# Optimization experiments

Measured on AMD Instinct MI355X. Metric: run time of the kernel, lower is better.

## Reference

```python
import math
import jax, jax.numpy as jnp
import numpy as np

B, S, D, H = 1, 4096, 1024, 16
HD = D // H


def setup_inputs() -> dict:
    key = jax.random.key(0)
    ks = jax.random.split(key, 11)
    s = 0.02
    inp = {
        "q": jax.random.normal(ks[0], (B, S, D), jnp.float32),
        "k": jax.random.normal(ks[1], (B, S, D), jnp.float32),
        "v": jax.random.normal(ks[2], (B, S, D), jnp.float32),
        # causal boolean mask, broadcastable over [B, H, S, S]
        "mask": jnp.tril(jnp.ones((S, S), jnp.bool_))[None, None],
        "Wq": jax.random.normal(ks[3], (D, D), jnp.float32) * s,
        "bq": jnp.zeros((D,), jnp.float32),
        "Wk": jax.random.normal(ks[4], (D, D), jnp.float32) * s,
        "bk": jnp.zeros((D,), jnp.float32),
        "Wv": jax.random.normal(ks[5], (D, D), jnp.float32) * s,
        "bv": jnp.zeros((D,), jnp.float32),
        "Wo": jax.random.normal(ks[6], (D, D), jnp.float32) * s,
        "bo": jnp.zeros((D,), jnp.float32),
    }
    return inp


def reference(q, k, v, mask, Wq, bq, Wk, bk, Wv, bv, Wo, bo):
    # projections (torch Linear: x @ W.T + b; here W is stored already transposed)
    qp = (q @ Wq + bq).reshape(B, S, H, HD)
    kp = (k @ Wk + bk).reshape(B, S, H, HD)
    vp = (v @ Wv + bv).reshape(B, S, H, HD)
    # scores: [B, H, S, S]
    scores = jnp.einsum("bqhd,bkhd->bhqk", qp, kp) / math.sqrt(HD)
    scores = jnp.where(mask, scores, -jnp.inf)
    attn = jax.nn.softmax(scores, axis=-1)
    # context: [B, H, S, HD] -> [B, S, D]
    ctx = jnp.einsum("bhqk,bkhd->bqhd", attn, vp).reshape(B, S, D)
    return ctx @ Wo + bo
```

## Files before the change

kernel.cpp:

```cpp
#include <hip/hip_runtime.h>
#include <hip/hip_bf16.h>


#define S_LEN 4096
#define D_DIM 1024
#define NHEAD 16
#define HDIM  64

typedef __hip_bfloat16 bf16;
typedef __attribute__((ext_vector_type(8))) short bf16x8v;
typedef __attribute__((ext_vector_type(4))) float f32x4;
typedef __attribute__((ext_vector_type(2))) unsigned int u32x2;

#define MFMA16(a, b, c) __builtin_amdgcn_mfma_f32_16x16x32_bf16((a), (b), (c), 0, 0, 0)

#if __has_builtin(__builtin_amdgcn_exp2f)
#define EXP2F(x) __builtin_amdgcn_exp2f(x)
#else
#define EXP2F(x) exp2f(x)
#endif

#define QSCALE (0.125f * 1.4426950408889634f)

__device__ __forceinline__ void async_cp16(const void* g, void* l) {
    __builtin_amdgcn_global_load_lds(
        (const __attribute__((address_space(1))) unsigned int*)g,
        (__attribute__((address_space(3))) unsigned int*)l, 16, 0, 0);
}

__device__ __forceinline__ unsigned int cvtpk_bf16(float lo, float hi) {
    unsigned int r;
    asm("v_cvt_pk_bf16_f32 %0, %1, %2" : "=v"(r) : "v"(lo), "v"(hi));
    return r;
}

__global__ __launch_bounds__(256) void cvt_bf16_k(
    const float* __restrict__ x0, const float* __restrict__ x1,
    const float* __restrict__ x2,
    bf16* __restrict__ y0, bf16* __restrict__ y1, bf16* __restrict__ y2)
{
    const float* x = (blockIdx.z == 0) ? x0 : (blockIdx.z == 1) ? x1 : x2;
    bf16*       y = (blockIdx.z == 0) ? y0 : (blockIdx.z == 1) ? y1 : y2;
    const size_t i = ((size_t)blockIdx.x * 256 + threadIdx.x);
    const float4 v = ((const float4*)x)[i];
    union { bf16 h[4]; short4 s; } u;
    u.h[0] = __float2bfloat16(v.x);
    u.h[1] = __float2bfloat16(v.y);
    u.h[2] = __float2bfloat16(v.z);
    u.h[3] = __float2bfloat16(v.w);
    ((short4*)y)[i] = u.s;
}

__global__ __launch_bounds__(256) void transpose_cvt_k(
    const float* __restrict__ W0, const float* __restrict__ W1,
    const float* __restrict__ W2, const float* __restrict__ W3,
    bf16* __restrict__ T0, bf16* __restrict__ T1,
    bf16* __restrict__ T2, bf16* __restrict__ T3)
{
    const float* W = (blockIdx.z == 0) ? W0 : (blockIdx.z == 1) ? W1
                   : (blockIdx.z == 2) ? W2 : W3;
    bf16*       Wt = (blockIdx.z == 0) ? T0 : (blockIdx.z == 1) ? T1
                   : (blockIdx.z == 2) ? T2 : T3;
    __shared__ float t[32][33];
    const int bx = blockIdx.x << 5, by = blockIdx.y << 5;
    const int tx = threadIdx.x & 31, ty = threadIdx.x >> 5;
#pragma unroll
    for (int i = 0; i < 32; i += 8)
        t[ty + i][tx] = W[(size_t)(by + ty + i) * D_DIM + bx + tx];
    __syncthreads();
#pragma unroll
    for (int i = 0; i < 32; i += 8)
        Wt[(size_t)(bx + ty + i) * D_DIM + by + tx] = __float2bfloat16(t[tx][ty + i]);
}

struct GemmJob {
    const bf16* A; const bf16* Wt; const float* bias; void* out;
    int mode; float scale;
};

__global__ __launch_bounds__(256) void gemm_k(GemmJob j0, GemmJob j1, GemmJob j2)
{
    const GemmJob j = (blockIdx.z == 0) ? j0 : (blockIdx.z == 1) ? j1 : j2;
    const int K = D_DIM;
    const int bn = blockIdx.x << 6;
    const int bm = blockIdx.y << 7;
    const int tid = threadIdx.x;
    const int w = tid >> 6, lane = tid & 63;
    const int col = lane & 15, g = lane >> 4;
    const int wr = (w >> 1) << 6, wc = (w & 1) << 5;

    __shared__ bf16 As[128 * 64];
    __shared__ bf16 Bs[64 * 64];

    f32x4 acc[4][2];
#pragma unroll
    for (int i = 0; i < 4; ++i)
#pragma unroll
        for (int jj = 0; jj < 2; ++jj) acc[i][jj] = (f32x4){0.f, 0.f, 0.f, 0.f};

    for (int kb = 0; kb < K; kb += 64) {
        __syncthreads();
#pragma unroll
        for (int e = 0; e < 4; ++e) {
            const int lin = (e << 8) + tid;
            const int row = lin >> 3, kc = lin & 7;
            async_cp16(j.A + (size_t)(bm + row) * K + kb + (kc << 3), &As[lin << 3]);
        }
#pragma unroll
        for (int e = 0; e < 2; ++e) {
            const int lin = (e << 8) + tid;
            const int row = lin >> 3, kc = lin & 7;
            async_cp16(j.Wt + (size_t)(bn + row) * K + kb + (kc << 3), &Bs[lin << 3]);
        }
        __syncthreads();

#pragma unroll
        for (int s = 0; s < 2; ++s) {
            bf16x8v af[4], bfv[2];
#pragma unroll
            for (int i = 0; i < 4; ++i)
                af[i] = *(const bf16x8v*)&As[((wr + (i << 4) + col) << 6) + (s << 5) + (g << 3)];
#pragma unroll
            for (int jj = 0; jj < 2; ++jj)
                bfv[jj] = *(const bf16x8v*)&Bs[((wc + (jj << 4) + col) << 6) + (s << 5) + (g << 3)];
#pragma unroll
            for (int i = 0; i < 4; ++i)
#pragma unroll
                for (int jj = 0; jj < 2; ++jj)
                    acc[i][jj] = MFMA16(af[i], bfv[jj], acc[i][jj]);
        }
    }

#pragma unroll
    for (int i = 0; i < 4; ++i)
#pragma unroll
    for (int jj = 0; jj < 2; ++jj)
#pragma unroll
    for (int reg = 0; reg < 4; ++reg) {
        const int row = bm + wr + (i << 4) + (g << 2) + reg;
        const int cg  = bn + wc + (jj << 4) + col;
        const float vv = (acc[i][jj][reg] + j.bias[cg]) * j.scale;
        if (j.mode == 0)
            ((bf16*)j.out)[(((size_t)(cg >> 6)) * S_LEN + row) * HDIM + (cg & 63)] =
                __float2bfloat16(vv);
        else if (j.mode == 2)
            ((bf16*)j.out)[((size_t)(cg >> 6) * HDIM + (cg & 63)) * S_LEN + row] =
                __float2bfloat16(vv);
        else
            ((float*)j.out)[(size_t)row * D_DIM + cg] = vv;
    }
}

__global__ __launch_bounds__(256) void attn_mfma_k(
    const bf16* __restrict__ Qp, const bf16* __restrict__ Kp,
    const bf16* __restrict__ Vt, bf16* __restrict__ ctx)
{
    __shared__ bf16 Ks[2][4096];
    __shared__ bf16 Vs[2][4096];

    const int bid = blockIdx.x;
    const int qb  = 31 - (bid >> 4);
    const int h   = bid & 15;
    const int q0  = qb << 7;
    const int tid = threadIdx.x, w = tid >> 6, lane = tid & 63;
    const int col = lane & 15, g = lane >> 4;

    const bf16* Kh = Kp + (size_t)h * S_LEN * HDIM;
    const bf16* Vh = Vt + (size_t)h * HDIM * S_LEN;

    const int qrowA = q0 + (w << 4) + col;
    const int qrowB = qrowA + 64;
    const size_t qbaseA = ((size_t)h * S_LEN + qrowA) * HDIM + (g << 3);
    const size_t qbaseB = qbaseA + (size_t)64 * HDIM;
    const bf16x8v qfA0 = *(const bf16x8v*)(Qp + qbaseA);
    const bf16x8v qfA1 = *(const bf16x8v*)(Qp + qbaseA + 32);
    const bf16x8v qfB0 = *(const bf16x8v*)(Qp + qbaseB);
    const bf16x8v qfB1 = *(const bf16x8v*)(Qp + qbaseB + 32);

    float plA = 0.f, plB = 0.f;
    f32x4 accA[4], accB[4];
#pragma unroll
    for (int t = 0; t < 4; ++t) {
        accA[t] = (f32x4){0.f, 0.f, 0.f, 0.f};
        accB[t] = (f32x4){0.f, 0.f, 0.f, 0.f};
    }

    const int nkb = (qb << 1) + 2;

    auto stage = [&](int buf, int kb) {
        const int kk0 = kb << 6;
#pragma unroll
        for (int e = 0; e < 2; ++e) {
            const int lin = (e << 8) + tid;
            const int t = lin >> 7, G = (lin >> 4) & 7, c = lin & 15;
            async_cp16(Kh + (size_t)(kk0 + (t << 4) + c) * HDIM + (G << 3),
                       &Ks[buf][lin << 3]);
            async_cp16(Vh + (size_t)((t << 4) + c) * S_LEN + kk0 + (G << 3),
                       &Vs[buf][lin << 3]);
        }
    };

    stage(0, 0);
    __syncthreads();

    for (int kb = 0; kb < nkb; ++kb) {
        const int cur = kb & 1;
        if (kb + 1 < nkb) stage(cur ^ 1, kb + 1);
        const int kk0 = kb << 6;
        const bf16* Kc = Ks[cur];
        const bf16* Vc = Vs[cur];

        f32x4 saA[4], saB[4];
#pragma unroll
        for (int t = 0; t < 4; ++t) {
            saA[t] = (f32x4){0.f, 0.f, 0.f, 0.f};
            saB[t] = (f32x4){0.f, 0.f, 0.f, 0.f};
        }
        __builtin_amdgcn_s_setprio(1);
#pragma unroll
        for (int t = 0; t < 4; ++t) {
            const bf16x8v kf0 = *(const bf16x8v*)&Kc[((t << 7) + (g << 4) + col) << 3];
            const bf16x8v kf1 = *(const bf16x8v*)&Kc[((t << 7) + 64 + (g << 4) + col) << 3];
            saA[t] = MFMA16(kf0, qfA0, saA[t]);
            saA[t] = MFMA16(kf1, qfA1, saA[t]);
            saB[t] = MFMA16(kf0, qfB0, saB[t]);
            saB[t] = MFMA16(kf1, qfB1, saB[t]);
        }
        __builtin_amdgcn_s_setprio(0);

        const bool maskt = (kb >= nkb - 2);
#pragma unroll
        for (int t = 0; t < 4; ++t) {
#pragma unroll
            for (int reg = 0; reg < 4; ++reg) {
                const int kidx = kk0 + (t << 4) + (g << 2) + reg;
                float pA, pB;
                if (maskt && kidx > qrowA) pA = 0.f;
                else                       pA = EXP2F(saA[t][reg]);
                if (maskt && kidx > qrowB) pB = 0.f;
                else                       pB = EXP2F(saB[t][reg]);
                plA += pA; saA[t][reg] = pA;
                plB += pB; saB[t][reg] = pB;
            }
        }

        union { unsigned int wd[4]; bf16x8v v; } pA0, pA1, pB0, pB1;
        {
            unsigned int c0[4], c1[4];
#pragma unroll
            for (int t = 0; t < 4; ++t) {
                c0[t] = cvtpk_bf16(saA[t][0], saA[t][1]);
                c1[t] = cvtpk_bf16(saA[t][2], saA[t][3]);
            }
            u32x2 r0 = __builtin_amdgcn_permlane32_swap(c0[0], c0[1], false, false);
            u32x2 r1 = __builtin_amdgcn_permlane32_swap(c1[0], c1[1], false, false);
            u32x2 s0 = __builtin_amdgcn_permlane16_swap(r0[0], r0[1], false, false);
            u32x2 s1 = __builtin_amdgcn_permlane16_swap(r1[0], r1[1], false, false);
            pA0.wd[0] = s0[0]; pA0.wd[1] = s1[0]; pA0.wd[2] = s0[1]; pA0.wd[3] = s1[1];
            r0 = __builtin_amdgcn_permlane32_swap(c0[2], c0[3], false, false);
            r1 = __builtin_amdgcn_permlane32_swap(c1[2], c1[3], false, false);
            s0 = __builtin_amdgcn_permlane16_swap(r0[0], r0[1], false, false);
            s1 = __builtin_amdgcn_permlane16_swap(r1[0], r1[1], false, false);
            pA1.wd[0] = s0[0]; pA1.wd[1] = s1[0]; pA1.wd[2] = s0[1]; pA1.wd[3] = s1[1];
        }
        {
            unsigned int c0[4], c1[4];
#pragma unroll
            for (int t = 0; t < 4; ++t) {
                c0[t] = cvtpk_bf16(saB[t][0], saB[t][1]);
                c1[t] = cvtpk_bf16(saB[t][2], saB[t][3]);
            }
            u32x2 r0 = __builtin_amdgcn_permlane32_swap(c0[0], c0[1], false, false);
            u32x2 r1 = __builtin_amdgcn_permlane32_swap(c1[0], c1[1], false, false);
            u32x2 s0 = __builtin_amdgcn_permlane16_swap(r0[0], r0[1], false, false);
            u32x2 s1 = __builtin_amdgcn_permlane16_swap(r1[0], r1[1], false, false);
            pB0.wd[0] = s0[0]; pB0.wd[1] = s1[0]; pB0.wd[2] = s0[1]; pB0.wd[3] = s1[1];
            r0 = __builtin_amdgcn_permlane32_swap(c0[2], c0[3], false, false);
            r1 = __builtin_amdgcn_permlane32_swap(c1[2], c1[3], false, false);
            s0 = __builtin_amdgcn_permlane16_swap(r0[0], r0[1], false, false);
            s1 = __builtin_amdgcn_permlane16_swap(r1[0], r1[1], false, false);
            pB1.wd[0] = s0[0]; pB1.wd[1] = s1[0]; pB1.wd[2] = s0[1]; pB1.wd[3] = s1[1];
        }

        __builtin_amdgcn_s_setprio(1);
#pragma unroll
        for (int t = 0; t < 4; ++t) {
            const bf16x8v vf0 = *(const bf16x8v*)&Vc[((t << 7) + (g << 4) + col) << 3];
            const bf16x8v vf1 = *(const bf16x8v*)&Vc[((t << 7) + 64 + (g << 4) + col) << 3];
            accA[t] = MFMA16(vf0, pA0.v, accA[t]);
            accA[t] = MFMA16(vf1, pA1.v, accA[t]);
            accB[t] = MFMA16(vf0, pB0.v, accB[t]);
            accB[t] = MFMA16(vf1, pB1.v, accB[t]);
        }
        __builtin_amdgcn_s_setprio(0);

        __syncthreads();
    }

    float lA = plA, lB = plB;
    lA += __shfl_xor(lA, 16); lA += __shfl_xor(lA, 32);
    lB += __shfl_xor(lB, 16); lB += __shfl_xor(lB, 32);
    const float invA = 1.f / lA;
    const float invB = 1.f / lB;

#pragma unroll
    for (int t = 0; t < 4; ++t) {
        union { bf16 hh[4]; short4 s4; } uA, uB;
#pragma unroll
        for (int reg = 0; reg < 4; ++reg) {
            uA.hh[reg] = __float2bfloat16(accA[t][reg] * invA);
            uB.hh[reg] = __float2bfloat16(accB[t][reg] * invB);
        }
        *(short4*)&ctx[(size_t)qrowA * D_DIM + h * HDIM + (t << 4) + (g << 2)] = uA.s4;
        *(short4*)&ctx[(size_t)qrowB * D_DIM + h * HDIM + (t << 4) + (g << 2)] = uB.s4;
    }
}

extern "C" void kernel_launch(void* const* d_in, const int* in_sizes, int n_in,
                              void* d_out, int out_size, void* d_ws, size_t ws_size,
                              hipStream_t stream)
{
    const float* q  = (const float*)d_in[0];
    const float* k  = (const float*)d_in[1];
    const float* v  = (const float*)d_in[2];
    const float* Wq = (const float*)d_in[4];
    const float* bq = (const float*)d_in[5];
    const float* Wk = (const float*)d_in[6];
    const float* bk = (const float*)d_in[7];
    const float* Wv = (const float*)d_in[8];
    const float* bv = (const float*)d_in[9];
    const float* Wo = (const float*)d_in[10];
    const float* bo = (const float*)d_in[11];

    const size_t PE  = (size_t)S_LEN * D_DIM;
    const size_t WTE = (size_t)D_DIM * D_DIM;

    const dim3 tg(32, 32, 4);
    const dim3 gg(D_DIM / 64, S_LEN / 128, 1);
    const dim3 gg3(D_DIM / 64, S_LEN / 128, 3);
    const dim3 cg((unsigned)(PE / 1024), 1, 3);

    if (ws_size >= (size_t)64 * 1024 * 1024) {
        bf16* Qb = (bf16*)d_ws;
        bf16* Kb = Qb + PE;
        bf16* Vb = Kb + PE;
        bf16* Qp = Vb + PE;
        bf16* Kp = Qp + PE;
        bf16* Vt = Kp + PE;
        bf16* Wtq = Vt + PE;
        bf16* Wtk = Wtq + WTE;
        bf16* Wtv = Wtk + WTE;
        bf16* Wto = Wtv + WTE;
        bf16* ctx = Qb;

        transpose_cvt_k<<<tg, 256, 0, stream>>>(Wq, Wk, Wv, Wo, Wtq, Wtk, Wtv, Wto);
        cvt_bf16_k<<<cg, 256, 0, stream>>>(q, k, v, Qb, Kb, Vb);

        GemmJob jq{Qb, Wtq, bq, Qp, 0, QSCALE};
        GemmJob jk{Kb, Wtk, bk, Kp, 0, 1.0f};
        GemmJob jv{Vb, Wtv, bv, Vt, 2, 1.0f};
        gemm_k<<<gg3, 256, 0, stream>>>(jq, jk, jv);

        attn_mfma_k<<<dim3(512), 256, 0, stream>>>(Qp, Kp, Vt, ctx);

        GemmJob jo{ctx, Wto, bo, d_out, 1, 1.0f};
        gemm_k<<<gg, 256, 0, stream>>>(jo, jo, jo);
    } else {
        bf16* X  = (bf16*)d_ws;
        bf16* Qp = X + PE;
        bf16* Kp = Qp + PE;
        bf16* Vt = Kp + PE;
        bf16* Wtq = Vt + PE;
        bf16* Wtk = Wtq + WTE;
        bf16* Wtv = Wtk + WTE;
        bf16* Wto = Wtv + WTE;

        transpose_cvt_k<<<tg, 256, 0, stream>>>(Wq, Wk, Wv, Wo, Wtq, Wtk, Wtv, Wto);

        const dim3 cg1((unsigned)(PE / 1024), 1, 1);
        cvt_bf16_k<<<cg1, 256, 0, stream>>>(q, q, q, X, X, X);
        GemmJob jq{X, Wtq, bq, Qp, 0, QSCALE};
        gemm_k<<<gg, 256, 0, stream>>>(jq, jq, jq);
        cvt_bf16_k<<<cg1, 256, 0, stream>>>(k, k, k, X, X, X);
        GemmJob jk{X, Wtk, bk, Kp, 0, 1.0f};
        gemm_k<<<gg, 256, 0, stream>>>(jk, jk, jk);
        cvt_bf16_k<<<cg1, 256, 0, stream>>>(v, v, v, X, X, X);
        GemmJob jv{X, Wtv, bv, Vt, 2, 1.0f};
        gemm_k<<<gg, 256, 0, stream>>>(jv, jv, jv);

        attn_mfma_k<<<dim3(512), 256, 0, stream>>>(Qp, Kp, Vt, X);

        GemmJob jo{X, Wto, bo, d_out, 1, 1.0f};
        gemm_k<<<gg, 256, 0, stream>>>(jo, jo, jo);
    }
}
```

Baseline: 347.7 us.

## Split long causal attention rows across two blocks and combine partials

Query blocks in the second half of the sequence (qb>=16) now have their key range split into two chunks, each handled by a separate workgroup, which raises the grid from 512 to 768 blocks. Partial unnormalised outputs and row sums go to fp32 scratch, and a new combine kernel adds them and normalises. The diagonal tile handling is also specialised so the fully masked A-half of the last tile skips its MFMAs. The aim is better load balance across CUs for the causal triangle, paid for with an extra launch and fp32 partial traffic. Partials skip max-subtraction, as the original code already did.

```diff
diff --git a/kernel.cpp b/kernel.cpp
--- a/kernel.cpp
+++ b/kernel.cpp
@@ -21,6 +21,8 @@
 #endif
 
 #define QSCALE (0.125f * 1.4426950408889634f)
+
+template<int N> struct IC { static constexpr int value = N; };
 
 __device__ __forceinline__ void async_cp16(const void* g, void* l) {
     __builtin_amdgcn_global_load_lds(
@@ -153,14 +155,26 @@
 
 __global__ __launch_bounds__(256) void attn_mfma_k(
     const bf16* __restrict__ Qp, const bf16* __restrict__ Kp,
-    const bf16* __restrict__ Vt, bf16* __restrict__ ctx)
+    const bf16* __restrict__ Vt, bf16* __restrict__ ctx,
+    float* __restrict__ Opart, float* __restrict__ lpart, int mode)
 {
     __shared__ bf16 Ks[2][4096];
     __shared__ bf16 Vs[2][4096];
 
     const int bid = blockIdx.x;
-    const int qb  = 31 - (bid >> 4);
     const int h   = bid & 15;
+    const int jid = bid >> 4;
+
+    int qb, t0, nt, chunk;
+    bool dosplit, hdiag;
+    if (mode == 1) {
+        if (jid < 16)      { qb = 31 - jid;        t0 = 2*qb - 30; nt = 32;        dosplit = true;  chunk = 1; hdiag = true;  }
+        else if (jid < 32) { qb = 31 - (jid - 16); t0 = 0;         nt = 2*qb - 30; dosplit = true;  chunk = 0; hdiag = false; }
+        else               { qb = 15 - (jid - 32); t0 = 0;         nt = 2*qb + 2;  dosplit = false; chunk = 0; hdiag = true;  }
+    } else {
+        qb = 31 - jid; t0 = 0; nt = 2*qb + 2; dosplit = false; chunk = 0; hdiag = true;
+    }
+
     const int q0  = qb << 7;
     const int tid = threadIdx.x, w = tid >> 6, lane = tid & 63;
     const int col = lane & 15, g = lane >> 4;
@@ -185,8 +199,6 @@
         accB[t] = (f32x4){0.f, 0.f, 0.f, 0.f};
     }
 
-    const int nkb = (qb << 1) + 2;
-
     auto stage = [&](int buf, int kb) {
         const int kk0 = kb << 6;
 #pragma unroll
@@ -200,12 +212,8 @@
         }
     };
 
-    stage(0, 0);
-    __syncthreads();
-
-    for (int kb = 0; kb < nkb; ++kb) {
-        const int cur = kb & 1;
-        if (kb + 1 < nkb) stage(cur ^ 1, kb + 1);
+    auto body = [&](auto mtag, int kb, int cur) {
+        constexpr int MODE = decltype(mtag)::value;
         const int kk0 = kb << 6;
         const bf16* Kc = Ks[cur];
         const bf16* Vc = Vs[cur];
@@ -221,31 +229,35 @@
         for (int t = 0; t < 4; ++t) {
             const bf16x8v kf0 = *(const bf16x8v*)&Kc[((t << 7) + (g << 4) + col) << 3];
             const bf16x8v kf1 = *(const bf16x8v*)&Kc[((t << 7) + 64 + (g << 4) + col) << 3];
-            saA[t] = MFMA16(kf0, qfA0, saA[t]);
-            saA[t] = MFMA16(kf1, qfA1, saA[t]);
+            if (MODE != 2) {
+                saA[t] = MFMA16(kf0, qfA0, saA[t]);
+                saA[t] = MFMA16(kf1, qfA1, saA[t]);
+            }
             saB[t] = MFMA16(kf0, qfB0, saB[t]);
             saB[t] = MFMA16(kf1, qfB1, saB[t]);
         }
         __builtin_amdgcn_s_setprio(0);
 
-        const bool maskt = (kb >= nkb - 2);
 #pragma unroll
         for (int t = 0; t < 4; ++t) {
 #pragma unroll
             for (int reg = 0; reg < 4; ++reg) {
                 const int kidx = kk0 + (t << 4) + (g << 2) + reg;
-                float pA, pB;
-                if (maskt && kidx > qrowA) pA = 0.f;
-                else                       pA = EXP2F(saA[t][reg]);
-                if (maskt && kidx > qrowB) pB = 0.f;
-                else                       pB = EXP2F(saB[t][reg]);
-                plA += pA; saA[t][reg] = pA;
+                if (MODE != 2) {
+                    float pA;
+                    if (MODE == 1 && kidx > qrowA) pA = 0.f;
+                    else                           pA = EXP2F(saA[t][reg]);
+                    plA += pA; saA[t][reg] = pA;
+                }
+                float pB;
+                if (MODE == 2 && kidx > qrowB) pB = 0.f;
+                else                           pB = EXP2F(saB[t][reg]);
                 plB += pB; saB[t][reg] = pB;
             }
         }
 
         union { unsigned int wd[4]; bf16x8v v; } pA0, pA1, pB0, pB1;
-        {
+        if (MODE != 2) {
             unsigned int c0[4], c1[4];
 #pragma unroll
             for (int t = 0; t < 4; ++t) {
@@ -287,33 +299,90 @@
         for (int t = 0; t < 4; ++t) {
             const bf16x8v vf0 = *(const bf16x8v*)&Vc[((t << 7) + (g << 4) + col) << 3];
             const bf16x8v vf1 = *(const bf16x8v*)&Vc[((t << 7) + 64 + (g << 4) + col) << 3];
-            accA[t] = MFMA16(vf0, pA0.v, accA[t]);
-            accA[t] = MFMA16(vf1, pA1.v, accA[t]);
+            if (MODE != 2) {
+                accA[t] = MFMA16(vf0, pA0.v, accA[t]);
+                accA[t] = MFMA16(vf1, pA1.v, accA[t]);
+            }
             accB[t] = MFMA16(vf0, pB0.v, accB[t]);
             accB[t] = MFMA16(vf1, pB1.v, accB[t]);
         }
         __builtin_amdgcn_s_setprio(0);
-
+    };
+
+    int kb = t0, cur = 0;
+    const int kend = t0 + nt;
+    stage(0, kb);
+    __syncthreads();
+
+    const int nmain = hdiag ? nt - 2 : nt;
+    for (int i = 0; i < nmain; ++i, ++kb) {
+        if (kb + 1 < kend) stage(cur ^ 1, kb + 1);
+        body(IC<0>{}, kb, cur);
         __syncthreads();
+        cur ^= 1;
+    }
+    if (hdiag) {
+        stage(cur ^ 1, kb + 1);
+        body(IC<1>{}, kb, cur);
+        __syncthreads();
+        cur ^= 1; ++kb;
+        body(IC<2>{}, kb, cur);
     }
 
     float lA = plA, lB = plB;
     lA += __shfl_xor(lA, 16); lA += __shfl_xor(lA, 32);
     lB += __shfl_xor(lB, 16); lB += __shfl_xor(lB, 32);
-    const float invA = 1.f / lA;
-    const float invB = 1.f / lB;
-
-#pragma unroll
-    for (int t = 0; t < 4; ++t) {
-        union { bf16 hh[4]; short4 s4; } uA, uB;
-#pragma unroll
-        for (int reg = 0; reg < 4; ++reg) {
-            uA.hh[reg] = __float2bfloat16(accA[t][reg] * invA);
-            uB.hh[reg] = __float2bfloat16(accB[t][reg] * invB);
-        }
-        *(short4*)&ctx[(size_t)qrowA * D_DIM + h * HDIM + (t << 4) + (g << 2)] = uA.s4;
-        *(short4*)&ctx[(size_t)qrowB * D_DIM + h * HDIM + (t << 4) + (g << 2)] = uB.s4;
-    }
+
+    if (!dosplit) {
+        const float invA = 1.f / lA;
+        const float invB = 1.f / lB;
+#pragma unroll
+        for (int t = 0; t < 4; ++t) {
+            union { bf16 hh[4]; short4 s4; } uA, uB;
+#pragma unroll
+            for (int reg = 0; reg < 4; ++reg) {
+                uA.hh[reg] = __float2bfloat16(accA[t][reg] * invA);
+                uB.hh[reg] = __float2bfloat16(accB[t][reg] * invB);
+            }
+            *(short4*)&ctx[(size_t)qrowA * D_DIM + h * HDIM + (t << 4) + (g << 2)] = uA.s4;
+            *(short4*)&ctx[(size_t)qrowB * D_DIM + h * HDIM + (t << 4) + (g << 2)] = uB.s4;
+        }
+    } else {
+        const int srowA = ((qb - 16) << 7) + (w << 4) + col;
+        const int srowB = srowA + 64;
+        float* OpA = Opart + (((size_t)chunk * NHEAD + h) * 2048 + srowA) * HDIM;
+        float* OpB = Opart + (((size_t)chunk * NHEAD + h) * 2048 + srowB) * HDIM;
+#pragma unroll
+        for (int t = 0; t < 4; ++t) {
+            *(f32x4*)&OpA[(t << 4) + (g << 2)] = accA[t];
+            *(f32x4*)&OpB[(t << 4) + (g << 2)] = accB[t];
+        }
+        if (g == 0) {
+            lpart[((size_t)chunk * NHEAD + h) * 2048 + srowA] = lA;
+            lpart[((size_t)chunk * NHEAD + h) * 2048 + srowB] = lB;
+        }
+    }
+}
+
+__global__ __launch_bounds__(256) void combine_k(
+    const float* __restrict__ Opart, const float* __restrict__ lpart,
+    bf16* __restrict__ ctx)
+{
+    const int tid = threadIdx.x;
+    const int row = (blockIdx.x << 4) + (tid >> 4);
+    const int d4  = (tid & 15) << 2;
+    const int h   = row >> 11;
+    const int srow = row & 2047;
+    const float4 a = *(const float4*)&Opart[(size_t)row * HDIM + d4];
+    const float4 b = *(const float4*)&Opart[(size_t)(32768 + row) * HDIM + d4];
+    const float inv = 1.f / (lpart[row] + lpart[32768 + row]);
+    union { bf16 hh[4]; short4 s4; } u;
+    u.hh[0] = __float2bfloat16((a.x + b.x) * inv);
+    u.hh[1] = __float2bfloat16((a.y + b.y) * inv);
+    u.hh[2] = __float2bfloat16((a.z + b.z) * inv);
+    u.hh[3] = __float2bfloat16((a.w + b.w) * inv);
+    const int qrow = 2048 + srow;
+    *(short4*)&ctx[(size_t)qrow * D_DIM + h * HDIM + d4] = u.s4;
 }
 
 extern "C" void kernel_launch(void* const* d_in, const int* in_sizes, int n_in,
@@ -352,6 +421,8 @@
         bf16* Wtv = Wtk + WTE;
         bf16* Wto = Wtv + WTE;
         bf16* ctx = Qb;
+        float* Opart = (float*)Kb;
+        float* lpart = (float*)(Wto + WTE);
 
         transpose_cvt_k<<<tg, 256, 0, stream>>>(Wq, Wk, Wv, Wo, Wtq, Wtk, Wtv, Wto);
         cvt_bf16_k<<<cg, 256, 0, stream>>>(q, k, v, Qb, Kb, Vb);
@@ -361,7 +432,8 @@
         GemmJob jv{Vb, Wtv, bv, Vt, 2, 1.0f};
         gemm_k<<<gg3, 256, 0, stream>>>(jq, jk, jv);
 
-        attn_mfma_k<<<dim3(512), 256, 0, stream>>>(Qp, Kp, Vt, ctx);
+        attn_mfma_k<<<dim3(768), 256, 0, stream>>>(Qp, Kp, Vt, ctx, Opart, lpart, 1);
+        combine_k<<<dim3(2048), 256, 0, stream>>>(Opart, lpart, ctx);
 
         GemmJob jo{ctx, Wto, bo, d_out, 1, 1.0f};
         gemm_k<<<gg, 256, 0, stream>>>(jo, jo, jo);
@@ -388,7 +460,7 @@
         GemmJob jv{X, Wtv, bv, Vt, 2, 1.0f};
         gemm_k<<<gg, 256, 0, stream>>>(jv, jv, jv);
 
-        attn_mfma_k<<<dim3(512), 256, 0, stream>>>(Qp, Kp, Vt, X);
+        attn_mfma_k<<<dim3(512), 256, 0, stream>>>(Qp, Kp, Vt, X, nullptr, nullptr, 0);
 
         GemmJob jo{X, Wto, bo, d_out, 1, 1.0f};
         gemm_k<<<gg, 256, 0, stream>>>(jo, jo, jo);
```

New measurement: 302.5 us. 13.0% less time.
